# Optimization experiments

Hardware: AMD Instinct MI355X
Metric: run time of the kernel (lower is better)

Reference implementation:

```python
import jax, jax.numpy as jnp
import numpy as np

B, SQ, SK, D = 32, 2048, 2048, 64


def setup_inputs() -> dict:
    key = jax.random.key(0)
    kq, kk, km = jax.random.split(key, 3)
    q = jax.random.normal(kq, (B, SQ, D), dtype=jnp.float32)
    k = jax.random.normal(kk, (B, SK, D), dtype=jnp.float32)
    mask = jax.random.randint(km, (B, SQ, SK), 0, 2, dtype=jnp.int32)
    return {"q": q, "k": k, "mask": mask}


def reference(q, k, mask):
    # scores = q @ k^T / sqrt(D)  -> [B, SQ, SK]
    scale = 1.0 / np.sqrt(q.shape[-1]).astype(np.float32)
    scores = jnp.einsum('bqd,bkd->bqk', q, k) * scale
    scores = jnp.where(mask == 0, -jnp.inf, scores)
    return jax.nn.softmax(scores, axis=-1)
```

## Files before the change

### kernel.cpp

```cpp
#include <hip/hip_runtime.h>
#include <math.h>

constexpr int BB  = 32;
constexpr int SQL = 2048;
constexpr int SKL = 2048;
constexpr int DD  = 64;

using f32x4 = __attribute__((ext_vector_type(4))) float;
using bfrag = __attribute__((ext_vector_type(8))) short;
typedef unsigned long long u64;

static __device__ __forceinline__ unsigned short f2bf(float x) {
    unsigned u = __float_as_uint(x);
    u = u + 0x7FFFu + ((u >> 16) & 1u);
    return (unsigned short)(u >> 16);
}
static __device__ __forceinline__ float bf2f(unsigned short h) {
    return __uint_as_float((unsigned)h << 16);
}

static __device__ __forceinline__ void gld16(const void* g, void* l) {
    __builtin_amdgcn_global_load_lds(
        (const __attribute__((address_space(1))) void*)(size_t)g,
        (__attribute__((address_space(3))) void*)(unsigned)(size_t)l,
        16, 0, 0);
}

__global__ __launch_bounds__(256) void split_k_swz(
    const float* __restrict__ k, unsigned char* __restrict__ kswz)
{
    const int i0 = blockIdx.x * blockDim.x + threadIdx.x;
    const int g  = i0 & 7;
    const int c  = (i0 >> 3) & 2047;
    const int b  = i0 >> 14;
    const float* kp = k + ((size_t)(b * 2048 + c)) * DD + g * 8;
    bfrag h, lo;
    #pragma unroll
    for (int j = 0; j < 8; ++j) {
        const float x = kp[j];
        const unsigned short hh = f2bf(x);
        h[j]  = (short)hh;
        lo[j] = (short)f2bf(x - bf2f(hh));
    }
    const int sw = (c & 7) << 4;
    unsigned char* rec = kswz + ((size_t)(b * 2048 + c)) * 256;
    *(bfrag*)(rec + ((g * 16) ^ sw))       = h;
    *(bfrag*)(rec + 128 + ((g * 16) ^ sw)) = lo;
}

#define MF(A, B, C) __builtin_amdgcn_mfma_f32_16x16x32_bf16((A), (B), (C), 0, 0, 0)

template<bool PRE>
__global__ __launch_bounds__(512, 4) void sdpa_v14(
    const float* __restrict__ q, const float* __restrict__ k,
    const int* __restrict__ mask, const unsigned char* __restrict__ kswz,
    u64* __restrict__ bits, float* __restrict__ out)
{
    __shared__ char kring[3 * 8192];
    __shared__ char mring[3 * 16384];

    const int t   = threadIdx.x;
    const int l   = t & 63;
    const int w   = t >> 6;
    const int lr  = l & 15;
    const int lg  = l >> 4;
    const int bid = blockIdx.x;
    const int swz = (bid & 7) * 64 + (bid >> 3);
    const int b   = swz >> 4;
    const int r0  = (swz & 15) * 128;
    const int R   = w * 16 + lr;
    const size_t rowg = (size_t)b * SQL + (size_t)(r0 + R);
    const int swk   = (lr & 7) << 4;
    const int koff0 = (lg * 16) ^ swk;
    const int koff1 = ((lg + 4) * 16) ^ swk;
    const int moff0 = R * 128 + ((lg ^ (R & 7)) << 4);
    const int moff1 = R * 128 + (((4 | lg) ^ (R & 7)) << 4);

    constexpr float QS = 0.18033688011112042f;
    bfrag qh0, ql0, qh1, ql1;
    {
        const float* qp = q + rowg * DD + lg * 8;
        const f32x4 x0 = *(const f32x4*)qp;
        const f32x4 x1 = *(const f32x4*)(qp + 4);
        const f32x4 y0 = *(const f32x4*)(qp + 32);
        const f32x4 y1 = *(const f32x4*)(qp + 36);
        #pragma unroll
        for (int j = 0; j < 4; ++j) {
            float a = x0[j] * QS, c = x1[j] * QS;
            float d = y0[j] * QS, e = y1[j] * QS;
            unsigned short h;
            h = f2bf(a); qh0[j]     = (short)h; ql0[j]     = (short)f2bf(a - bf2f(h));
            h = f2bf(c); qh0[j + 4] = (short)h; ql0[j + 4] = (short)f2bf(c - bf2f(h));
            h = f2bf(d); qh1[j]     = (short)h; ql1[j]     = (short)f2bf(d - bf2f(h));
            h = f2bf(e); qh1[j + 4] = (short)h; ql1[j + 4] = (short)f2bf(e - bf2f(h));
        }
    }

    const char*  kstg = PRE ? (const char*)kswz + ((size_t)b * SKL) * 256 + t * 16 : nullptr;
    const float* kraw = PRE ? nullptr : k + (size_t)b * SKL * DD;
    const char* mstgA = (const char*)mask
        + ((size_t)b * SQL + (size_t)(r0 + (t >> 3))) * (SKL * 4)
        + (size_t)(((t & 7) ^ ((t >> 3) & 7)) << 4);
    const char* mstgB = mstgA + (size_t)64 * (SKL * 4);
    u64*  bitsp = PRE ? bits + ((size_t)bid * 512 + t) * 8 : nullptr;
    const int* mdir = mask + rowg * SKL + lg * 4;
    float* outp = out + rowg * SKL + lg * 4;

    const int cvc   = t >> 4;
    const int cvd   = t & 15;
    const int cvrec = cvc * 256 + (((cvd >> 1) * 16) ^ ((cvc & 7) << 4)) + (cvd & 1) * 8;

#define STAGE_B(TT)                                                            \
  do {                                                                         \
    char* _kd = kring + sl * 8192;                                             \
    if constexpr (PRE) {                                                       \
      gld16(kstg + (size_t)(TT) * 8192, _kd + t * 16);                         \
    } else {                                                                   \
      const float* _kp = kraw + (size_t)((TT) * 32 + cvc) * 64 + cvd * 4;      \
      const f32x4 _v = *(const f32x4*)_kp;                                     \
      short4 _hi, _lo;                                                         \
      { unsigned short _t2;                                                    \
        _t2 = f2bf(_v[0]); _hi.x = (short)_t2; _lo.x = (short)f2bf(_v[0] - bf2f(_t2)); \
        _t2 = f2bf(_v[1]); _hi.y = (short)_t2; _lo.y = (short)f2bf(_v[1] - bf2f(_t2)); \
        _t2 = f2bf(_v[2]); _hi.z = (short)_t2; _lo.z = (short)f2bf(_v[2] - bf2f(_t2)); \
        _t2 = f2bf(_v[3]); _hi.w = (short)_t2; _lo.w = (short)f2bf(_v[3] - bf2f(_t2)); } \
      *(short4*)(_kd + cvrec)       = _hi;                                     \
      *(short4*)(_kd + cvrec + 128) = _lo;                                     \
    }                                                                          \
  } while (0)

#define STAGE_A(TT)                                                            \
  do {                                                                         \
    STAGE_B(TT);                                                               \
    char* _md = mring + sl * 16384;                                            \
    gld16(mstgA + (size_t)(TT) * 128, _md + t * 16);                           \
    gld16(mstgB + (size_t)(TT) * 128, _md + 8192 + t * 16);                    \
  } while (0)

#define FRAGS                                                                  \
    const char* _kc = kring + sl * 8192 + lr * 256;                            \
    const bfrag _kh0 = *(const bfrag*)(_kc + koff0);                           \
    const bfrag _kh1 = *(const bfrag*)(_kc + koff1);                           \
    const bfrag _kl0 = *(const bfrag*)(_kc + 128 + koff0);                     \
    const bfrag _kl1 = *(const bfrag*)(_kc + 128 + koff1);                     \
    const bfrag _jh0 = *(const bfrag*)(_kc + 4096 + koff0);                    \
    const bfrag _jh1 = *(const bfrag*)(_kc + 4096 + koff1);                    \
    const bfrag _jl0 = *(const bfrag*)(_kc + 4096 + 128 + koff0);              \
    const bfrag _jl1 = *(const bfrag*)(_kc + 4096 + 128 + koff1);

#define MMAS                                                                   \
    f32x4 _h0 = {0.f,0.f,0.f,0.f}, _x0 = {0.f,0.f,0.f,0.f};                    \
    f32x4 _h1 = {0.f,0.f,0.f,0.f}, _x1 = {0.f,0.f,0.f,0.f};                    \
    _h0 = MF(_kh0, qh0, _h0);  _x0 = MF(_kh0, ql0, _x0);                       \
    _h0 = MF(_kh1, qh1, _h0);  _x0 = MF(_kl0, qh0, _x0);                       \
    _x0 = MF(_kh1, ql1, _x0);  _x0 = MF(_kl1, qh1, _x0);                       \
    _h1 = MF(_jh0, qh0, _h1);  _x1 = MF(_jh0, ql0, _x1);                       \
    _h1 = MF(_jh1, qh1, _h1);  _x1 = MF(_jl0, qh0, _x1);                       \
    _x1 = MF(_jh1, ql1, _x1);  _x1 = MF(_jl1, qh1, _x1);                       \
    const f32x4 _s0 = _h0 + _x0;                                               \
    const f32x4 _s1 = _h1 + _x1;

#define NIB4(M) ((unsigned)((M).x ? 1u:0u) | ((M).y ? 2u:0u) |                 \
                 ((M).z ? 4u:0u) | ((M).w ? 8u:0u))

#define STEP_A(TT, VP, VN, SH, DOSTAGE)                                        \
  do {                                                                         \
    if constexpr (PRE) { asm volatile("s_waitcnt vmcnt(" #VP ")" ::: "memory"); } \
    else { asm volatile("s_waitcnt vmcnt(" #VN ") lgkmcnt(0)" ::: "memory"); } \
    __builtin_amdgcn_sched_barrier(0);                                         \
    __builtin_amdgcn_s_barrier();                                              \
    __builtin_amdgcn_sched_barrier(0);                                         \
    FRAGS                                                                      \
    const char* _mb = mring + sl * 16384;                                      \
    const int4 _m0 = *(const int4*)(_mb + moff0);                              \
    const int4 _m1 = *(const int4*)(_mb + moff1);                              \
    asm volatile("s_waitcnt lgkmcnt(0)" ::: "memory");                         \
    __builtin_amdgcn_sched_barrier(0);                                         \
    MMAS                                                                       \
    const unsigned _n0 = NIB4(_m0);                                            \
    const unsigned _n1 = NIB4(_m1);                                            \
    psum += ((_n0 & 1u) ? exp2f(_s0[0]) : 0.f) + ((_n0 & 2u) ? exp2f(_s0[1]) : 0.f) \
          + ((_n0 & 4u) ? exp2f(_s0[2]) : 0.f) + ((_n0 & 8u) ? exp2f(_s0[3]) : 0.f) \
          + ((_n1 & 1u) ? exp2f(_s1[0]) : 0.f) + ((_n1 & 2u) ? exp2f(_s1[1]) : 0.f) \
          + ((_n1 & 4u) ? exp2f(_s1[2]) : 0.f) + ((_n1 & 8u) ? exp2f(_s1[3]) : 0.f); \
    bv |= ((u64)(_n0 | (_n1 << 4))) << (SH);                                   \
    __builtin_amdgcn_sched_barrier(0);                                         \
    __builtin_amdgcn_s_barrier();                                              \
    __builtin_amdgcn_sched_barrier(0);                                         \
    if (DOSTAGE) { STAGE_A((TT) + 3); }                                        \
    sl = (sl == 2) ? 0 : sl + 1;                                               \
  } while (0)

#define STEP_B(TT, VP, SH, DOSTAGE)                                            \
  do {                                                                         \
    if constexpr (PRE) { asm volatile("s_waitcnt vmcnt(" #VP ")" ::: "memory"); } \
    else { asm volatile("s_waitcnt lgkmcnt(0)" ::: "memory"); }                \
    __builtin_amdgcn_sched_barrier(0);                                         \
    __builtin_amdgcn_s_barrier();                                              \
    __builtin_amdgcn_sched_barrier(0);                                         \
    FRAGS                                                                      \
    asm volatile("s_waitcnt lgkmcnt(0)" ::: "memory");                         \
    __builtin_amdgcn_sched_barrier(0);                                         \
    MMAS                                                                       \
    unsigned _n0, _n1;                                                         \
    if constexpr (PRE) {                                                       \
        _n0 = (unsigned)(bq >> (SH)) & 0xFu;                                   \
        _n1 = (unsigned)(bq >> ((SH) + 4)) & 0xFu;                             \
    } else {                                                                   \
        const int4 _m0 = *(const int4*)(mdir + (TT) * 32);                     \
        const int4 _m1 = *(const int4*)(mdir + (TT) * 32 + 16);                \
        _n0 = NIB4(_m0); _n1 = NIB4(_m1);                                      \
    }                                                                          \
    f32x4 _o0, _o1;                                                            \
    _o0[0] = (_n0 & 1u) ? exp2f(_s0[0]) * rinv : 0.f;                          \
    _o0[1] = (_n0 & 2u) ? exp2f(_s0[1]) * rinv : 0.f;                          \
    _o0[2] = (_n0 & 4u) ? exp2f(_s0[2]) * rinv : 0.f;                          \
    _o0[3] = (_n0 & 8u) ? exp2f(_s0[3]) * rinv : 0.f;                          \
    _o1[0] = (_n1 & 1u) ? exp2f(_s1[0]) * rinv : 0.f;                          \
    _o1[1] = (_n1 & 2u) ? exp2f(_s1[1]) * rinv : 0.f;                          \
    _o1[2] = (_n1 & 4u) ? exp2f(_s1[2]) * rinv : 0.f;                          \
    _o1[3] = (_n1 & 8u) ? exp2f(_s1[3]) * rinv : 0.f;                          \
    *(f32x4*)(outp + (TT) * 32)      = _o0;                                    \
    *(f32x4*)(outp + (TT) * 32 + 16) = _o1;                                    \
    __builtin_amdgcn_sched_barrier(0);                                         \
    __builtin_amdgcn_s_barrier();                                              \
    __builtin_amdgcn_sched_barrier(0);                                         \
    if (DOSTAGE) { STAGE_B((TT) + 3); }                                        \
    sl = (sl == 2) ? 0 : sl + 1;                                               \
  } while (0)

    int sl;
    float psum = 0.f;
    u64 bv = 0;
    sl = 0; STAGE_A(0);
    sl = 1; STAGE_A(1);
    sl = 2; STAGE_A(2);
    sl = 0;

    for (int jg = 0; jg < 7; ++jg) {
        const int T0 = jg * 8;
        bv = 0;
        STEP_A(T0 + 0, 6, 4, 0,  1);
        STEP_A(T0 + 1, 6, 4, 8,  1);
        STEP_A(T0 + 2, 6, 4, 16, 1);
        STEP_A(T0 + 3, 6, 4, 24, 1);
        STEP_A(T0 + 4, 6, 4, 32, 1);
        STEP_A(T0 + 5, 6, 4, 40, 1);
        STEP_A(T0 + 6, 6, 4, 48, 1);
        STEP_A(T0 + 7, 6, 4, 56, 1);
        if constexpr (PRE) bitsp[jg] = bv;
    }
    bv = 0;
    STEP_A(56, 6, 4, 0,  1);
    STEP_A(57, 6, 4, 8,  1);
    STEP_A(58, 6, 4, 16, 1);
    STEP_A(59, 6, 4, 24, 1);
    STEP_A(60, 6, 4, 32, 1);
    STEP_A(61, 6, 4, 40, 0);
    STEP_A(62, 3, 2, 48, 0);
    STEP_A(63, 0, 0, 56, 0);
    if constexpr (PRE) bitsp[7] = bv;

    psum += __shfl_xor(psum, 16, 64);
    psum += __shfl_xor(psum, 32, 64);
    const float rinv = 1.0f / psum;

    u64 bq = 0, bvn = 0;
    if constexpr (PRE) bq = bitsp[0];
    sl = 0; STAGE_B(0);
    sl = 1; STAGE_B(1);
    sl = 2; STAGE_B(2);
    sl = 0;

    STEP_B(0, 2, 0, 1);
    if constexpr (PRE) bvn = bitsp[1];
    STEP_B(1, 4, 8,  1);
    STEP_B(2, 6, 16, 1);
    STEP_B(3, 6, 24, 1);
    STEP_B(4, 6, 32, 1);
    STEP_B(5, 6, 40, 1);
    STEP_B(6, 6, 48, 1);
    STEP_B(7, 6, 56, 1);
    bq = bvn;
    for (int jg = 1; jg < 7; ++jg) {
        const int T0 = jg * 8;
        STEP_B(T0 + 0, 6, 0, 1);
        if constexpr (PRE) bvn = bitsp[jg + 1];
        STEP_B(T0 + 1, 6, 8,  1);
        STEP_B(T0 + 2, 6, 16, 1);
        STEP_B(T0 + 3, 6, 24, 1);
        STEP_B(T0 + 4, 6, 32, 1);
        STEP_B(T0 + 5, 6, 40, 1);
        STEP_B(T0 + 6, 6, 48, 1);
        STEP_B(T0 + 7, 6, 56, 1);
        bq = bvn;
    }
    STEP_B(56, 6, 0,  1);
    STEP_B(57, 6, 8,  1);
    STEP_B(58, 6, 16, 1);
    STEP_B(59, 6, 24, 1);
    STEP_B(60, 6, 32, 1);
    STEP_B(61, 6, 40, 0);
    STEP_B(62, 5, 48, 0);
    STEP_B(63, 4, 56, 0);

#undef STEP_B
#undef STEP_A
#undef NIB4
#undef MMAS
#undef FRAGS
#undef STAGE_A
#undef STAGE_B
}

extern "C" void kernel_launch(void* const* d_in, const int* in_sizes, int n_in,
                              void* d_out, int out_size, void* d_ws, size_t ws_size,
                              hipStream_t stream) {
    const float* q    = (const float*)d_in[0];
    const float* k    = (const float*)d_in[1];
    const int*   mask = (const int*)d_in[2];
    float*       out  = (float*)d_out;

    const size_t KS_B   = (size_t)BB * SKL * 256;
    const size_t BITS_B = (size_t)512 * 512 * 8 * 8;

    if (ws_size >= KS_B + BITS_B) {
        unsigned char* ksp = (unsigned char*)d_ws;
        u64* bitsp = (u64*)((char*)d_ws + KS_B);
        split_k_swz<<<2048, 256, 0, stream>>>(k, ksp);
        sdpa_v14<true><<<512, 512, 0, stream>>>(q, k, mask, ksp, bitsp, out);
    } else {
        sdpa_v14<false><<<512, 512, 0, stream>>>(q, k, mask, nullptr, nullptr, out);
    }
}
```

Baseline: 363.4 us.

## Load mask directly to registers with prefetch and keep mask bits in LDS

Replaces the LDS ring staging of the int mask with direct per-lane register loads prefetched two tiles ahead. The per-row mask bitmask produced in the first pass is now kept in shared memory instead of a global workspace buffer. The aim is to cut LDS traffic and footprint plus the global round trip for the bits. The cost is more vector registers for in-flight mask loads and less latency hiding through the shared ring.

```diff
diff --git a/kernel.cpp b/kernel.cpp
--- a/kernel.cpp
+++ b/kernel.cpp
@@ -49,15 +49,20 @@
 }
 
 #define MF(A, B, C) __builtin_amdgcn_mfma_f32_16x16x32_bf16((A), (B), (C), 0, 0, 0)
+#define WAITV(N) asm volatile("s_waitcnt vmcnt(" #N ")" ::: "memory")
+#define WAITL    asm volatile("s_waitcnt lgkmcnt(0)" ::: "memory")
+#define SBAR     __builtin_amdgcn_s_barrier()
+#define SCHED    __builtin_amdgcn_sched_barrier(0)
+#define ADV      sl = (sl == 2) ? 0 : sl + 1
 
 template<bool PRE>
-__global__ __launch_bounds__(512, 4) void sdpa_v14(
+__global__ __launch_bounds__(512, 4) void sdpa_v15(
     const float* __restrict__ q, const float* __restrict__ k,
     const int* __restrict__ mask, const unsigned char* __restrict__ kswz,
-    u64* __restrict__ bits, float* __restrict__ out)
+    float* __restrict__ out)
 {
     __shared__ char kring[3 * 8192];
-    __shared__ char mring[3 * 16384];
+    __shared__ u64  bitlds[512][8];
 
     const int t   = threadIdx.x;
     const int l   = t & 63;
@@ -73,8 +78,6 @@
     const int swk   = (lr & 7) << 4;
     const int koff0 = (lg * 16) ^ swk;
     const int koff1 = ((lg + 4) * 16) ^ swk;
-    const int moff0 = R * 128 + ((lg ^ (R & 7)) << 4);
-    const int moff1 = R * 128 + (((4 | lg) ^ (R & 7)) << 4);
 
     constexpr float QS = 0.18033688011112042f;
     bfrag qh0, ql0, qh1, ql1;
@@ -95,22 +98,18 @@
             h = f2bf(e); qh1[j + 4] = (short)h; ql1[j + 4] = (short)f2bf(e - bf2f(h));
         }
     }
-
-    const char*  kstg = PRE ? (const char*)kswz + ((size_t)b * SKL) * 256 + t * 16 : nullptr;
+    SCHED;
+
+    const char*  kstg = PRE ? (const char*)kswz + (size_t)b * SKL * 256 + t * 16 : nullptr;
     const float* kraw = PRE ? nullptr : k + (size_t)b * SKL * DD;
-    const char* mstgA = (const char*)mask
-        + ((size_t)b * SQL + (size_t)(r0 + (t >> 3))) * (SKL * 4)
-        + (size_t)(((t & 7) ^ ((t >> 3) & 7)) << 4);
-    const char* mstgB = mstgA + (size_t)64 * (SKL * 4);
-    u64*  bitsp = PRE ? bits + ((size_t)bid * 512 + t) * 8 : nullptr;
-    const int* mdir = mask + rowg * SKL + lg * 4;
-    float* outp = out + rowg * SKL + lg * 4;
+    const int*   mdir = mask + rowg * SKL + lg * 4;
+    float*       outp = out + rowg * SKL + lg * 4;
 
     const int cvc   = t >> 4;
     const int cvd   = t & 15;
     const int cvrec = cvc * 256 + (((cvd >> 1) * 16) ^ ((cvc & 7) << 4)) + (cvd & 1) * 8;
 
-#define STAGE_B(TT)                                                            \
+#define STAGE(TT)                                                              \
   do {                                                                         \
     char* _kd = kring + sl * 8192;                                             \
     if constexpr (PRE) {                                                       \
@@ -129,14 +128,6 @@
     }                                                                          \
   } while (0)
 
-#define STAGE_A(TT)                                                            \
-  do {                                                                         \
-    STAGE_B(TT);                                                               \
-    char* _md = mring + sl * 16384;                                            \
-    gld16(mstgA + (size_t)(TT) * 128, _md + t * 16);                           \
-    gld16(mstgB + (size_t)(TT) * 128, _md + 8192 + t * 16);                    \
-  } while (0)
-
 #define FRAGS                                                                  \
     const char* _kc = kring + sl * 8192 + lr * 256;                            \
     const bfrag _kh0 = *(const bfrag*)(_kc + koff0);                           \
@@ -163,54 +154,40 @@
 #define NIB4(M) ((unsigned)((M).x ? 1u:0u) | ((M).y ? 2u:0u) |                 \
                  ((M).z ? 4u:0u) | ((M).w ? 8u:0u))
 
-#define STEP_A(TT, VP, VN, SH, DOSTAGE)                                        \
+#define STEP_A(TT, VMC, M0, M1, SH, DOSTAGE, DOMASK)                           \
   do {                                                                         \
-    if constexpr (PRE) { asm volatile("s_waitcnt vmcnt(" #VP ")" ::: "memory"); } \
-    else { asm volatile("s_waitcnt vmcnt(" #VN ") lgkmcnt(0)" ::: "memory"); } \
-    __builtin_amdgcn_sched_barrier(0);                                         \
-    __builtin_amdgcn_s_barrier();                                              \
-    __builtin_amdgcn_sched_barrier(0);                                         \
+    if constexpr (PRE) { WAITV(VMC); }                                         \
+    else { asm volatile("s_waitcnt vmcnt(0) lgkmcnt(0)" ::: "memory"); }       \
+    SCHED; SBAR; SCHED;                                                        \
     FRAGS                                                                      \
-    const char* _mb = mring + sl * 16384;                                      \
-    const int4 _m0 = *(const int4*)(_mb + moff0);                              \
-    const int4 _m1 = *(const int4*)(_mb + moff1);                              \
-    asm volatile("s_waitcnt lgkmcnt(0)" ::: "memory");                         \
-    __builtin_amdgcn_sched_barrier(0);                                         \
+    WAITL; SCHED;                                                              \
     MMAS                                                                       \
-    const unsigned _n0 = NIB4(_m0);                                            \
-    const unsigned _n1 = NIB4(_m1);                                            \
+    const unsigned _n0 = NIB4(M0);                                             \
+    const unsigned _n1 = NIB4(M1);                                             \
     psum += ((_n0 & 1u) ? exp2f(_s0[0]) : 0.f) + ((_n0 & 2u) ? exp2f(_s0[1]) : 0.f) \
           + ((_n0 & 4u) ? exp2f(_s0[2]) : 0.f) + ((_n0 & 8u) ? exp2f(_s0[3]) : 0.f) \
           + ((_n1 & 1u) ? exp2f(_s1[0]) : 0.f) + ((_n1 & 2u) ? exp2f(_s1[1]) : 0.f) \
           + ((_n1 & 4u) ? exp2f(_s1[2]) : 0.f) + ((_n1 & 8u) ? exp2f(_s1[3]) : 0.f); \
     bv |= ((u64)(_n0 | (_n1 << 4))) << (SH);                                   \
-    __builtin_amdgcn_sched_barrier(0);                                         \
-    __builtin_amdgcn_s_barrier();                                              \
-    __builtin_amdgcn_sched_barrier(0);                                         \
-    if (DOSTAGE) { STAGE_A((TT) + 3); }                                        \
-    sl = (sl == 2) ? 0 : sl + 1;                                               \
+    SCHED; SBAR; SCHED;                                                        \
+    if (DOSTAGE) { STAGE((TT) + 3); }                                          \
+    if (DOMASK) {                                                              \
+        M0 = *(const int4*)(mdir + ((TT) + 2) * 32);                           \
+        M1 = *(const int4*)(mdir + ((TT) + 2) * 32 + 16);                      \
+    }                                                                          \
+    ADV;                                                                       \
   } while (0)
 
-#define STEP_B(TT, VP, SH, DOSTAGE)                                            \
+#define STEP_B(TT, VMC, SH, DOSTAGE)                                           \
   do {                                                                         \
-    if constexpr (PRE) { asm volatile("s_waitcnt vmcnt(" #VP ")" ::: "memory"); } \
-    else { asm volatile("s_waitcnt lgkmcnt(0)" ::: "memory"); }                \
-    __builtin_amdgcn_sched_barrier(0);                                         \
-    __builtin_amdgcn_s_barrier();                                              \
-    __builtin_amdgcn_sched_barrier(0);                                         \
+    if constexpr (PRE) { WAITV(VMC); }                                         \
+    else { asm volatile("s_waitcnt vmcnt(0) lgkmcnt(0)" ::: "memory"); }       \
+    SCHED; SBAR; SCHED;                                                        \
     FRAGS                                                                      \
-    asm volatile("s_waitcnt lgkmcnt(0)" ::: "memory");                         \
-    __builtin_amdgcn_sched_barrier(0);                                         \
+    WAITL; SCHED;                                                              \
     MMAS                                                                       \
-    unsigned _n0, _n1;                                                         \
-    if constexpr (PRE) {                                                       \
-        _n0 = (unsigned)(bq >> (SH)) & 0xFu;                                   \
-        _n1 = (unsigned)(bq >> ((SH) + 4)) & 0xFu;                             \
-    } else {                                                                   \
-        const int4 _m0 = *(const int4*)(mdir + (TT) * 32);                     \
-        const int4 _m1 = *(const int4*)(mdir + (TT) * 32 + 16);                \
-        _n0 = NIB4(_m0); _n1 = NIB4(_m1);                                      \
-    }                                                                          \
+    const unsigned _n0 = (unsigned)(bq >> (SH)) & 0xFu;                        \
+    const unsigned _n1 = (unsigned)(bq >> ((SH) + 4)) & 0xFu;                  \
     f32x4 _o0, _o1;                                                            \
     _o0[0] = (_n0 & 1u) ? exp2f(_s0[0]) * rinv : 0.f;                          \
     _o0[1] = (_n0 & 2u) ? exp2f(_s0[1]) * rinv : 0.f;                          \
@@ -222,58 +199,68 @@
     _o1[3] = (_n1 & 8u) ? exp2f(_s1[3]) * rinv : 0.f;                          \
     *(f32x4*)(outp + (TT) * 32)      = _o0;                                    \
     *(f32x4*)(outp + (TT) * 32 + 16) = _o1;                                    \
-    __builtin_amdgcn_sched_barrier(0);                                         \
-    __builtin_amdgcn_s_barrier();                                              \
-    __builtin_amdgcn_sched_barrier(0);                                         \
-    if (DOSTAGE) { STAGE_B((TT) + 3); }                                        \
-    sl = (sl == 2) ? 0 : sl + 1;                                               \
+    SCHED; SBAR; SCHED;                                                        \
+    if (DOSTAGE) { STAGE((TT) + 3); }                                          \
+    ADV;                                                                       \
   } while (0)
 
-    int sl;
+    int sl = 0;
     float psum = 0.f;
     u64 bv = 0;
-    sl = 0; STAGE_A(0);
-    sl = 1; STAGE_A(1);
-    sl = 2; STAGE_A(2);
-    sl = 0;
-
-    for (int jg = 0; jg < 7; ++jg) {
+    STAGE(0); ADV;
+    STAGE(1); ADV;
+    STAGE(2); ADV;
+    int4 me0 = *(const int4*)(mdir);
+    int4 me1 = *(const int4*)(mdir + 16);
+    int4 mo0 = *(const int4*)(mdir + 32);
+    int4 mo1 = *(const int4*)(mdir + 48);
+
+    bv = 0;
+    STEP_A(0, 2, me0, me1, 0,  1, 1);
+    STEP_A(1, 3, mo0, mo1, 8,  1, 1);
+    STEP_A(2, 3, me0, me1, 16, 1, 1);
+    STEP_A(3, 3, mo0, mo1, 24, 1, 1);
+    STEP_A(4, 3, me0, me1, 32, 1, 1);
+    STEP_A(5, 3, mo0, mo1, 40, 1, 1);
+    STEP_A(6, 3, me0, me1, 48, 1, 1);
+    STEP_A(7, 3, mo0, mo1, 56, 1, 1);
+    bitlds[t][0] = bv;
+
+    for (int jg = 1; jg < 7; ++jg) {
         const int T0 = jg * 8;
         bv = 0;
-        STEP_A(T0 + 0, 6, 4, 0,  1);
-        STEP_A(T0 + 1, 6, 4, 8,  1);
-        STEP_A(T0 + 2, 6, 4, 16, 1);
-        STEP_A(T0 + 3, 6, 4, 24, 1);
-        STEP_A(T0 + 4, 6, 4, 32, 1);
-        STEP_A(T0 + 5, 6, 4, 40, 1);
-        STEP_A(T0 + 6, 6, 4, 48, 1);
-        STEP_A(T0 + 7, 6, 4, 56, 1);
-        if constexpr (PRE) bitsp[jg] = bv;
-    }
+        STEP_A(T0 + 0, 3, me0, me1, 0,  1, 1);
+        STEP_A(T0 + 1, 3, mo0, mo1, 8,  1, 1);
+        STEP_A(T0 + 2, 3, me0, me1, 16, 1, 1);
+        STEP_A(T0 + 3, 3, mo0, mo1, 24, 1, 1);
+        STEP_A(T0 + 4, 3, me0, me1, 32, 1, 1);
+        STEP_A(T0 + 5, 3, mo0, mo1, 40, 1, 1);
+        STEP_A(T0 + 6, 3, me0, me1, 48, 1, 1);
+        STEP_A(T0 + 7, 3, mo0, mo1, 56, 1, 1);
+        bitlds[t][jg] = bv;
+    }
+
     bv = 0;
-    STEP_A(56, 6, 4, 0,  1);
-    STEP_A(57, 6, 4, 8,  1);
-    STEP_A(58, 6, 4, 16, 1);
-    STEP_A(59, 6, 4, 24, 1);
-    STEP_A(60, 6, 4, 32, 1);
-    STEP_A(61, 6, 4, 40, 0);
-    STEP_A(62, 3, 2, 48, 0);
-    STEP_A(63, 0, 0, 56, 0);
-    if constexpr (PRE) bitsp[7] = bv;
+    STEP_A(56, 3, me0, me1, 0,  1, 1);
+    STEP_A(57, 3, mo0, mo1, 8,  1, 1);
+    STEP_A(58, 3, me0, me1, 16, 1, 1);
+    STEP_A(59, 3, mo0, mo1, 24, 1, 1);
+    STEP_A(60, 3, me0, me1, 32, 1, 1);
+    STEP_A(61, 3, mo0, mo1, 40, 0, 1);
+    STEP_A(62, 2, me0, me1, 48, 0, 0);
+    STEP_A(63, 0, mo0, mo1, 56, 0, 0);
+    bitlds[t][7] = bv;
 
     psum += __shfl_xor(psum, 16, 64);
     psum += __shfl_xor(psum, 32, 64);
     const float rinv = 1.0f / psum;
 
-    u64 bq = 0, bvn = 0;
-    if constexpr (PRE) bq = bitsp[0];
-    sl = 0; STAGE_B(0);
-    sl = 1; STAGE_B(1);
-    sl = 2; STAGE_B(2);
-    sl = 0;
-
-    STEP_B(0, 2, 0, 1);
-    if constexpr (PRE) bvn = bitsp[1];
+    u64 bq = bitlds[t][0];
+    STAGE(0); ADV;
+    STAGE(1); ADV;
+    STAGE(2); ADV;
+
+    STEP_B(0, 2, 0,  1);
     STEP_B(1, 4, 8,  1);
     STEP_B(2, 6, 16, 1);
     STEP_B(3, 6, 24, 1);
@@ -281,11 +268,11 @@
     STEP_B(5, 6, 40, 1);
     STEP_B(6, 6, 48, 1);
     STEP_B(7, 6, 56, 1);
-    bq = bvn;
+
     for (int jg = 1; jg < 7; ++jg) {
+        bq = bitlds[t][jg];
         const int T0 = jg * 8;
-        STEP_B(T0 + 0, 6, 0, 1);
-        if constexpr (PRE) bvn = bitsp[jg + 1];
+        STEP_B(T0 + 0, 6, 0,  1);
         STEP_B(T0 + 1, 6, 8,  1);
         STEP_B(T0 + 2, 6, 16, 1);
         STEP_B(T0 + 3, 6, 24, 1);
@@ -293,8 +280,9 @@
         STEP_B(T0 + 5, 6, 40, 1);
         STEP_B(T0 + 6, 6, 48, 1);
         STEP_B(T0 + 7, 6, 56, 1);
-        bq = bvn;
-    }
+    }
+
+    bq = bitlds[t][7];
     STEP_B(56, 6, 0,  1);
     STEP_B(57, 6, 8,  1);
     STEP_B(58, 6, 16, 1);
@@ -309,8 +297,7 @@
 #undef NIB4
 #undef MMAS
 #undef FRAGS
-#undef STAGE_A
-#undef STAGE_B
+#undef STAGE
 }
 
 extern "C" void kernel_launch(void* const* d_in, const int* in_sizes, int n_in,
@@ -321,15 +308,13 @@
     const int*   mask = (const int*)d_in[2];
     float*       out  = (float*)d_out;
 
-    const size_t KS_B   = (size_t)BB * SKL * 256;
-    const size_t BITS_B = (size_t)512 * 512 * 8 * 8;
-
-    if (ws_size >= KS_B + BITS_B) {
+    const size_t KS_B = (size_t)BB * SKL * 256;
+
+    if (ws_size >= KS_B) {
         unsigned char* ksp = (unsigned char*)d_ws;
-        u64* bitsp = (u64*)((char*)d_ws + KS_B);
         split_k_swz<<<2048, 256, 0, stream>>>(k, ksp);
-        sdpa_v14<true><<<512, 512, 0, stream>>>(q, k, mask, ksp, bitsp, out);
+        sdpa_v15<true><<<512, 512, 0, stream>>>(q, k, mask, ksp, out);
     } else {
-        sdpa_v14<false><<<512, 512, 0, stream>>>(q, k, mask, nullptr, nullptr, out);
-    }
-}
+        sdpa_v15<false><<<512, 512, 0, stream>>>(q, k, mask, nullptr, out);
+    }
+}
```

Measured after the change: 359.4 us. About the same (-1.1%).
